# Performance work log

Measured on AMD Instinct MI355X. Metric: run time of the kernel, lower is better.

Reference implementation:

```python
import jax, jax.numpy as jnp
import numpy as np

BS, K, DIM = 16384, 1000, 768
GAMMA = 1.0


def setup_inputs() -> dict:
    key = jax.random.key(0)
    k1, k2, k3 = jax.random.split(key, 3)
    # one-hot mask selecting one semantic dipole per sample
    idx = jax.random.randint(k1, (BS,), 0, K)
    support_sets_mask = jax.nn.one_hot(idx, K, dtype=jnp.float32)
    # z: points on the unit sphere S^{dim-1}
    z = jax.random.normal(k2, (BS, DIM), dtype=jnp.float32)
    z = z / jnp.linalg.norm(z, axis=1, keepdims=True)
    # SUPPORT_SETS = semantic_dipoles_features reshaped to [K, 2*dim] (unit CLIP features per pole)
    sdf = jax.random.normal(k3, (K, 2, DIM), dtype=jnp.float32)
    sdf = sdf / jnp.linalg.norm(sdf, axis=2, keepdims=True)
    SUPPORT_SETS = sdf.reshape(K, 2 * DIM)
    # ALPHAS[k] = [1, -1]; LOGGAMMA = log(gamma) * ones
    ALPHAS = jnp.tile(jnp.array([1.0, -1.0], dtype=jnp.float32), (K, 1))
    LOGGAMMA = jnp.full((K, 2), np.log(GAMMA), dtype=jnp.float32)
    return {"support_sets_mask": support_sets_mask, "z": z,
            "SUPPORT_SETS": SUPPORT_SETS, "ALPHAS": ALPHAS, "LOGGAMMA": LOGGAMMA}


def reference(support_sets_mask, z, SUPPORT_SETS, ALPHAS, LOGGAMMA):
    bs, dim = z.shape
    # select dipole params per sample via mask matmuls
    support_sets_batch = (support_sets_mask @ SUPPORT_SETS).reshape(bs, 2, dim)  # [bs,2,dim]
    alphas_batch = (support_sets_mask @ ALPHAS)[:, :, None]                      # [bs,2,1]
    gammas_batch = jnp.exp(support_sets_mask @ LOGGAMMA)[:, :, None]             # [bs,2,1]
    # RBF gradient field: grad_f = -2 * sum_j alpha_j * gamma_j * exp(-gamma_j ||z - s_j||^2) * (z - s_j)
    D = z[:, None, :] - support_sets_batch                                       # [bs,2,dim]
    sq_norm = jnp.sum(D * D, axis=2, keepdims=True)                              # [bs,2,1]
    grad_f = -2.0 * jnp.sum(alphas_batch * gammas_batch * jnp.exp(-gammas_batch * sq_norm) * D, axis=1)  # [bs,dim]
    # tangent-space projection onto T_z S^{n}: (I - z z^T) w == w - (z.w) z  (rank-1 form)
    proj = grad_f - jnp.sum(z * grad_f, axis=1, keepdims=True) * z
    # normalize
    return proj / jnp.linalg.norm(proj, axis=1, keepdims=True)
```

## Files before the change

### kernel.cpp

```cpp
#include <hip/hip_runtime.h>


constexpr int K   = 1000;
constexpr int DIM = 768;
constexpr int VPR = K / 4;

typedef float f4 __attribute__((ext_vector_type(4)));

__global__ __launch_bounds__(256) void css_idx_kernel(
    const f4* __restrict__ mask4, int* __restrict__ idx, int bs)
{
    const int b    = (blockIdx.x * blockDim.x + threadIdx.x) >> 6;
    const int lane = threadIdx.x & 63;
    if (b >= bs) return;

    const f4* mrow = mask4 + (size_t)b * VPR;
    int found = -1;
    #pragma unroll 1
    for (int i = 0; i < 4; ++i) {
        const int e = i * 64 + lane;
        if (e < VPR) {
            f4 v = __builtin_nontemporal_load(mrow + e);
            if (v.x != 0.f) found = e * 4 + 0;
            if (v.y != 0.f) found = e * 4 + 1;
            if (v.z != 0.f) found = e * 4 + 2;
            if (v.w != 0.f) found = e * 4 + 3;
        }
        if (__ballot(found >= 0)) break;
    }
    #pragma unroll
    for (int off = 1; off < 64; off <<= 1)
        found = max(found, __shfl_xor(found, off, 64));
    if (lane == 0) idx[b] = found;
}

__global__ __launch_bounds__(256) void css_main_kernel(
    const int*   __restrict__ idx,
    const float* __restrict__ z,
    const float* __restrict__ ss,
    const float* __restrict__ alphas,
    const float* __restrict__ loggamma,
    float* __restrict__ out,
    int bs)
{
    const int gid  = blockIdx.x * blockDim.x + threadIdx.x;
    const int b    = gid >> 6;
    const int lane = threadIdx.x & 63;
    if (b >= bs) return;

    const f4* zrow = (const f4*)(z + (size_t)b * DIM);
    f4 z4[3];
    #pragma unroll
    for (int i = 0; i < 3; ++i) z4[i] = zrow[lane + i * 64];

    int k = idx[b];
    k = (k < 0) ? 0 : (k >= K ? K - 1 : k);

    const float a0  = alphas[2 * k];
    const float a1  = alphas[2 * k + 1];
    const float lg0 = loggamma[2 * k];
    const float lg1 = loggamma[2 * k + 1];

    const f4* srow = (const f4*)(ss + (size_t)k * (2 * DIM));

    f4 d0[3], d1[3];
    float sqn0 = 0.f, sqn1 = 0.f, zd0 = 0.f, zd1 = 0.f, d01 = 0.f, zsq = 0.f;
    #pragma unroll
    for (int i = 0; i < 3; ++i) {
        f4 s0 = srow[lane + i * 64];
        f4 s1 = srow[192 + lane + i * 64];
        d0[i] = z4[i] - s0;
        d1[i] = z4[i] - s1;
        sqn0 += d0[i].x*d0[i].x + d0[i].y*d0[i].y + d0[i].z*d0[i].z + d0[i].w*d0[i].w;
        sqn1 += d1[i].x*d1[i].x + d1[i].y*d1[i].y + d1[i].z*d1[i].z + d1[i].w*d1[i].w;
        zd0  += z4[i].x*d0[i].x + z4[i].y*d0[i].y + z4[i].z*d0[i].z + z4[i].w*d0[i].w;
        zd1  += z4[i].x*d1[i].x + z4[i].y*d1[i].y + z4[i].z*d1[i].z + z4[i].w*d1[i].w;
        d01  += d0[i].x*d1[i].x + d0[i].y*d1[i].y + d0[i].z*d1[i].z + d0[i].w*d1[i].w;
        zsq  += z4[i].x*z4[i].x + z4[i].y*z4[i].y + z4[i].z*z4[i].z + z4[i].w*z4[i].w;
    }
    #pragma unroll
    for (int off = 1; off < 64; off <<= 1) {
        sqn0 += __shfl_xor(sqn0, off, 64);
        sqn1 += __shfl_xor(sqn1, off, 64);
        zd0  += __shfl_xor(zd0,  off, 64);
        zd1  += __shfl_xor(zd1,  off, 64);
        d01  += __shfl_xor(d01,  off, 64);
        zsq  += __shfl_xor(zsq,  off, 64);
    }

    const float g0 = expf(lg0);
    const float g1 = expf(lg1);
    const float c0 = -2.f * a0 * g0 * expf(-g0 * sqn0);
    const float c1 = -2.f * a1 * g1 * expf(-g1 * sqn1);
    const float dot    = c0 * zd0 + c1 * zd1;
    const float gradsq = c0*c0*sqn0 + 2.f*c0*c1*d01 + c1*c1*sqn1;
    const float nsq    = gradsq - 2.f*dot*dot + dot*dot*zsq;
    const float inv    = 1.f / sqrtf(nsq);

    f4* orow = (f4*)(out + (size_t)b * DIM);
    #pragma unroll
    for (int i = 0; i < 3; ++i) {
        f4 r = (c0 * d0[i] + c1 * d1[i] - dot * z4[i]) * inv;
        __builtin_nontemporal_store(r, orow + lane + i * 64);
    }
}

extern "C" void kernel_launch(void* const* d_in, const int* in_sizes, int n_in,
                              void* d_out, int out_size, void* d_ws, size_t ws_size,
                              hipStream_t stream) {
    const float* mask     = (const float*)d_in[0];
    const float* z        = (const float*)d_in[1];
    const float* ss       = (const float*)d_in[2];
    const float* alphas   = (const float*)d_in[3];
    const float* loggamma = (const float*)d_in[4];
    float* out = (float*)d_out;
    int*   idx = (int*)d_ws;

    const int bs = in_sizes[1] / DIM;

    const int k1_blocks = (bs + 3) / 4;
    css_idx_kernel<<<k1_blocks, 256, 0, stream>>>((const f4*)mask, idx, bs);

    const int k2_blocks = (bs + 3) / 4;
    css_main_kernel<<<k2_blocks, 256, 0, stream>>>(idx, z, ss, alphas, loggamma, out, bs);
}
```

Before: 154.3 us.

## Fuse mask index search into main kernel and issue z loads early

Merges the one-hot index search and the RBF gradient kernel into a single launch. This removes the workspace index round-trip and the second kernel launch. The wave finds its row index from the ballot of lane hits and broadcasts it as a scalar. The z row is now loaded before the mask scan so its latency overlaps the search. The z row stays in registers during the scan, which may raise register pressure.

```diff
diff --git a/kernel.cpp b/kernel.cpp
--- a/kernel.cpp
+++ b/kernel.cpp
@@ -7,12 +7,24 @@
 
 typedef float f4 __attribute__((ext_vector_type(4)));
 
-__global__ __launch_bounds__(256) void css_idx_kernel(
-    const f4* __restrict__ mask4, int* __restrict__ idx, int bs)
+__global__ __launch_bounds__(256) void css_fused_kernel(
+    const f4*    __restrict__ mask4,
+    const float* __restrict__ z,
+    const float* __restrict__ ss,
+    const float* __restrict__ alphas,
+    const float* __restrict__ loggamma,
+    float*       __restrict__ out,
+    int bs)
 {
     const int b    = (blockIdx.x * blockDim.x + threadIdx.x) >> 6;
     const int lane = threadIdx.x & 63;
     if (b >= bs) return;
+
+    const f4* zrow = (const f4*)(z + (size_t)b * DIM);
+    f4 z4[3];
+    #pragma unroll
+    for (int i = 0; i < 3; ++i)
+        z4[i] = __builtin_nontemporal_load(zrow + lane + i * 64);
 
     const f4* mrow = mask4 + (size_t)b * VPR;
     int found = -1;
@@ -28,33 +40,11 @@
         }
         if (__ballot(found >= 0)) break;
     }
-    #pragma unroll
-    for (int off = 1; off < 64; off <<= 1)
-        found = max(found, __shfl_xor(found, off, 64));
-    if (lane == 0) idx[b] = found;
-}
-
-__global__ __launch_bounds__(256) void css_main_kernel(
-    const int*   __restrict__ idx,
-    const float* __restrict__ z,
-    const float* __restrict__ ss,
-    const float* __restrict__ alphas,
-    const float* __restrict__ loggamma,
-    float* __restrict__ out,
-    int bs)
-{
-    const int gid  = blockIdx.x * blockDim.x + threadIdx.x;
-    const int b    = gid >> 6;
-    const int lane = threadIdx.x & 63;
-    if (b >= bs) return;
-
-    const f4* zrow = (const f4*)(z + (size_t)b * DIM);
-    f4 z4[3];
-    #pragma unroll
-    for (int i = 0; i < 3; ++i) z4[i] = zrow[lane + i * 64];
-
-    int k = idx[b];
+    const unsigned long long hit = __ballot(found >= 0);
+    int k = 0;
+    if (hit) k = __shfl(found, (int)__ffsll(hit) - 1, 64);
     k = (k < 0) ? 0 : (k >= K ? K - 1 : k);
+    k = __builtin_amdgcn_readfirstlane(k);
 
     const float a0  = alphas[2 * k];
     const float a1  = alphas[2 * k + 1];
@@ -114,13 +104,10 @@
     const float* alphas   = (const float*)d_in[3];
     const float* loggamma = (const float*)d_in[4];
     float* out = (float*)d_out;
-    int*   idx = (int*)d_ws;
 
     const int bs = in_sizes[1] / DIM;
 
-    const int k1_blocks = (bs + 3) / 4;
-    css_idx_kernel<<<k1_blocks, 256, 0, stream>>>((const f4*)mask, idx, bs);
-
-    const int k2_blocks = (bs + 3) / 4;
-    css_main_kernel<<<k2_blocks, 256, 0, stream>>>(idx, z, ss, alphas, loggamma, out, bs);
+    const int blocks = (bs + 3) / 4;
+    css_fused_kernel<<<blocks, 256, 0, stream>>>(
+        (const f4*)mask, z, ss, alphas, loggamma, out, bs);
 }
```

Result: no change. 155.6 us (+0.9%).
